# Performance work log

Measured on AMD Instinct MI355X. Metric: run time of the kernel, lower is better.

The kernel has to match this reference:

```python
import jax, jax.numpy as jnp
import numpy as np

N_NODES = 8000
N_EDGES = 64000
HEADS = 8
OUT_C = 512
NEG_SLOPE = 0.2
EPS = 1e-16


def setup_inputs() -> dict:
    key = jax.random.key(0)
    ks = jax.random.split(key, 8)
    x = jax.random.normal(ks[0], (N_NODES, 128), dtype=jnp.float32)
    edge_index = jax.random.randint(ks[1], (2, N_EDGES), 0, N_NODES, dtype=jnp.int64)
    W_gat = jax.random.normal(ks[2], (128, HEADS * OUT_C), dtype=jnp.float32) * 0.05
    b_gat = jax.random.normal(ks[3], (HEADS * OUT_C,), dtype=jnp.float32) * 0.05
    att_src = jax.random.normal(ks[4], (HEADS, OUT_C), dtype=jnp.float32) * 0.05
    att_dst = jax.random.normal(ks[5], (HEADS, OUT_C), dtype=jnp.float32) * 0.05
    W_lin = jax.random.normal(ks[6], (HEADS * OUT_C, 512), dtype=jnp.float32) * 0.02
    b_lin = jax.random.normal(ks[7], (512,), dtype=jnp.float32) * 0.02
    return {"x": x, "edge_index": edge_index, "W_gat": W_gat, "b_gat": b_gat,
            "att_src": att_src, "att_dst": att_dst, "W_lin": W_lin, "b_lin": b_lin}


def reference(x, edge_index, W_gat, b_gat, att_src, att_dst, W_lin, b_lin):
    N = x.shape[0]
    # shared linear projection (PyG GATConv single-tensor input): [N, H, C]
    h = (x @ W_gat).reshape(N, HEADS, OUT_C)
    # add self loops (PyG default add_self_loops=True)
    loop = jnp.arange(N, dtype=edge_index.dtype)
    src = jnp.concatenate([edge_index[0], loop])  # source j
    dst = jnp.concatenate([edge_index[1], loop])  # destination i
    # per-node attention logits: [N, H]
    a_src = jnp.einsum('nhc,hc->nh', h, att_src)
    a_dst = jnp.einsum('nhc,hc->nh', h, att_dst)
    # edge logits, leaky relu
    e = jax.nn.leaky_relu(a_src[src] + a_dst[dst], NEG_SLOPE)  # [E, H]
    # softmax over edges sharing a destination
    emax = jax.ops.segment_max(e, dst, num_segments=N)
    ez = jnp.exp(e - emax[dst])
    denom = jax.ops.segment_sum(ez, dst, num_segments=N)
    alpha = ez / (denom[dst] + EPS)  # [E, H]
    # weighted scatter-add of source features
    msg = h[src] * alpha[:, :, None]  # [E, H, C]
    agg = jax.ops.segment_sum(msg, dst, num_segments=N)  # [N, H, C]
    gat_out = agg.reshape(N, HEADS * OUT_C) + b_gat
    return gat_out @ W_lin + b_lin
```

## Files before the change

kernel.cpp:

```cpp
#include <hip/hip_runtime.h>
#include <hip/hip_bf16.h>

#define NN   8000
#define NE   64000
#define NE2  72000
#define NH   8
#define OC   512
#define HC   4096
#define KIN  128
#define NOUT 512
#define YW   1024
#define MAXDEG 64
#define NEG_SLOPE 0.2f

#define VSRC_NB   128
#define PHA_NB    129

#define PB_GEMM_NB 64
#define FILL_BASE  64
#define BEFF_BASE  346
#define ATT_BASE   362
#define PHB_NB     862

#define GEMM_NB   500

using bf16 = __hip_bfloat16;
typedef float  f32x4  __attribute__((ext_vector_type(4)));
typedef __bf16 bf16x8 __attribute__((ext_vector_type(8)));

static __device__ __forceinline__ void gld_lds16(const bf16* g, bf16* l){
    __builtin_amdgcn_global_load_lds(
        (const __attribute__((address_space(1))) unsigned int*)g,
        (__attribute__((address_space(3))) unsigned int*)l, 16, 0, 0);
}

struct Acc24 { f32x4 a[2][4]; };

static __device__ __forceinline__ void gemm64x128_bk64(
    const bf16* __restrict__ A, int lda, const bf16* __restrict__ BT, int ldb,
    int K, bf16* sA, bf16* sB, int tid, Acc24& acc)
{
    const int lane = tid & 63;
    const int w    = tid >> 6;
    const int wm   = w >> 1, wn = w & 1;
    const int m16  = lane & 15, q = lane >> 4;

    const int cA0 = tid,        cA1 = tid + 256;
    const int rA0 = cA0 >> 3,   jA0 = (cA0 & 7) ^ (rA0 & 7);
    const int rA1 = cA1 >> 3,   jA1 = (cA1 & 7) ^ (rA1 & 7);
    const size_t gA0 = (size_t)rA0 * lda + jA0 * 8;
    const size_t gA1 = (size_t)rA1 * lda + jA1 * 8;
    size_t gB[4]; int cB[4];
    #pragma unroll
    for (int u=0; u<4; ++u){
        int c = tid + 256*u;
        int r = c >> 3, j = (c & 7) ^ (r & 7);
        cB[u] = c;
        gB[u] = (size_t)r * ldb + j * 8;
    }

    #pragma unroll
    for (int i=0;i<2;++i)
        #pragma unroll
        for (int j=0;j<4;++j)
            #pragma unroll
            for (int r=0;r<4;++r) acc.a[i][j][r] = 0.f;

    gld_lds16(A  + gA0, sA + cA0*8);
    gld_lds16(A  + gA1, sA + cA1*8);
    #pragma unroll
    for (int u=0; u<4; ++u) gld_lds16(BT + gB[u], sB + cB[u]*8);
    __syncthreads();

    const int nIter = K / 64;
    for (int it = 0; it < nIter; ++it){
        const int cur = it & 1, nxt = cur ^ 1;
        bf16x8 af[2][2], bfr[4][2];
        #pragma unroll
        for (int ks=0; ks<2; ++ks){
            #pragma unroll
            for (int i=0;i<2;++i){
                int row = wm*32 + i*16 + m16;
                int p   = (ks*4 + q) ^ (row & 7);
                af[i][ks] = *(const bf16x8*)(const void*)(sA + cur*64*64 + row*64 + p*8);
            }
            #pragma unroll
            for (int j=0;j<4;++j){
                int row = wn*64 + j*16 + m16;
                int p   = (ks*4 + q) ^ (row & 7);
                bfr[j][ks] = *(const bf16x8*)(const void*)(sB + cur*128*64 + row*64 + p*8);
            }
        }
        if (it + 1 < nIter){
            const size_t ko = (size_t)(it+1) * 64;
            gld_lds16(A  + gA0 + ko, sA + nxt*64*64 + cA0*8);
            gld_lds16(A  + gA1 + ko, sA + nxt*64*64 + cA1*8);
            #pragma unroll
            for (int u=0; u<4; ++u) gld_lds16(BT + gB[u] + ko, sB + nxt*128*64 + cB[u]*8);
        }
        #pragma unroll
        for (int ks=0; ks<2; ++ks)
            #pragma unroll
            for (int i=0;i<2;++i)
                #pragma unroll
                for (int j=0;j<4;++j)
                    acc.a[i][j] = __builtin_amdgcn_mfma_f32_16x16x32_bf16(af[i][ks], bfr[j][ks], acc.a[i][j], 0, 0, 0);
        __syncthreads();
    }
}

__global__ __launch_bounds__(256) void k_phaseA(
    const float* __restrict__ W_gat,
    const float* __restrict__ att_src, const float* __restrict__ att_dst,
    bf16* __restrict__ Wg, float* __restrict__ v,
    int* __restrict__ cursors)
{
    const int bid = blockIdx.x;
    const int tid = threadIdx.x;

    if (bid < VSRC_NB){
        int k = bid;
        int lane = tid & 63, g = tid >> 6;
        for (int hh = g; hh < NH; hh += 4){
            const float* wp = W_gat + (size_t)k*HC + hh*OC;
            bf16*        wb = Wg    + (size_t)k*HC + hh*OC;
            const float* as = att_src + hh*OC;
            const float* ad = att_dst + hh*OC;
            float ss = 0.f, sd = 0.f;
            #pragma unroll
            for (int c0=0; c0<OC; c0+=64){
                float wv = wp[c0+lane];
                wb[c0+lane] = __float2bfloat16(wv);
                ss = fmaf(wv, as[c0+lane], ss);
                sd = fmaf(wv, ad[c0+lane], sd);
            }
            #pragma unroll
            for (int off=32; off; off>>=1){
                ss += __shfl_down(ss, off);
                sd += __shfl_down(sd, off);
            }
            if (lane == 0){
                v[k*16 + hh]     = ss;
                v[k*16 + 8 + hh] = sd;
            }
        }
    } else {
        for (int i = tid*4; i < NN; i += 1024){
            int4 z; z.x = z.y = z.z = z.w = 0;
            *reinterpret_cast<int4*>(cursors + i) = z;
        }
    }
}

__global__ __launch_bounds__(256) void k_phaseB(
    const bf16* __restrict__ Wg, const float* __restrict__ W_lin,
    const float* __restrict__ b_gat, const int* __restrict__ eidx,
    bf16* __restrict__ WcT, float* __restrict__ beff_part,
    int* __restrict__ cursors, int* __restrict__ esrc,
    const float* __restrict__ x, const float* __restrict__ v,
    float* __restrict__ a_src, float* __restrict__ a_dst)
{
    __shared__ __align__(16) char smem_raw[16*132*2*4];
    const int bid = blockIdx.x;
    const int tid = threadIdx.x;

    if (bid < PB_GEMM_NB){
        bf16* sA = (bf16*)smem_raw;
        bf16* sB = (bf16*)smem_raw + 64*32;

        const int head = bid >> 3;
        const int rem  = bid & 7;
        const int m0   = (rem >> 2) * 64;
        const int n0   = (rem & 3) * 128;
        const int lane = tid & 63;
        const int w = tid >> 6, wm = w >> 1, wn = w & 1;
        const int m16 = lane & 15, q = lane >> 4;

        const int rA = tid >> 2, kA = (tid & 3) * 8;
        const bf16* Abase = Wg + (size_t)(m0 + rA)*HC + head*OC + kA;

        f32x4 acc[2][4];
        #pragma unroll
        for (int i=0;i<2;++i)
            #pragma unroll
            for (int j=0;j<4;++j)
                #pragma unroll
                for (int r=0;r<4;++r) acc[i][j][r] = 0.f;

        for (int kc = 0; kc < OC; kc += 32){
            __syncthreads();
            gld_lds16(Abase + kc, sA + tid*8);
            #pragma unroll
            for (int u=0; u<4; ++u){
                int idx = tid*4 + u;
                int r    = idx >> 5;
                int gcol = (idx & 31) * 4;
                const float* src = W_lin + (size_t)(head*OC + kc + r)*NOUT + n0 + gcol;
                float4 vv = *(const float4*)src;
                sB[(gcol+0)*32 + r] = __float2bfloat16(vv.x);
                sB[(gcol+1)*32 + r] = __float2bfloat16(vv.y);
                sB[(gcol+2)*32 + r] = __float2bfloat16(vv.z);
                sB[(gcol+3)*32 + r] = __float2bfloat16(vv.w);
            }
            __syncthreads();
            bf16x8 af[2], bfr[4];
            #pragma unroll
            for (int i=0;i<2;++i)
                af[i]  = *(const bf16x8*)(const void*)(sA + ((wm*32 + i*16 + m16)*32 + q*8));
            #pragma unroll
            for (int j=0;j<4;++j)
                bfr[j] = *(const bf16x8*)(const void*)(sB + ((wn*64 + j*16 + m16)*32 + q*8));
            #pragma unroll
            for (int i=0;i<2;++i)
                #pragma unroll
                for (int j=0;j<4;++j)
                    acc[i][j] = __builtin_amdgcn_mfma_f32_16x16x32_bf16(af[i], bfr[j], acc[i][j], 0, 0, 0);
        }

        #pragma unroll
        for (int i=0;i<2;++i){
            int row_base = m0 + wm*32 + i*16 + q*4;
            #pragma unroll
            for (int j=0;j<4;++j){
                int col = n0 + wn*64 + j*16 + m16;
                ushort4 pk;
                bf16 b0 = __float2bfloat16(acc[i][j][0]);
                bf16 b1 = __float2bfloat16(acc[i][j][1]);
                bf16 b2 = __float2bfloat16(acc[i][j][2]);
                bf16 b3 = __float2bfloat16(acc[i][j][3]);
                pk.x = *(unsigned short*)&b0; pk.y = *(unsigned short*)&b1;
                pk.z = *(unsigned short*)&b2; pk.w = *(unsigned short*)&b3;
                *reinterpret_cast<ushort4*>(WcT + (size_t)col*YW + head*KIN + row_base) = pk;
            }
        }
        return;
    }

    if (bid < BEFF_BASE){
        int e = (bid - FILL_BASE)*256 + tid;
        if (e < NE2){
            int src, dst;
            if (e < NE){ src = eidx[e]; dst = eidx[NE+e]; } else { src = dst = e - NE; }
            int pos = atomicAdd(&cursors[dst], 1);
            if (pos < MAXDEG) esrc[dst*MAXDEG + pos] = src;
        }
        return;
    }

    if (bid < ATT_BASE){
        int b = bid - BEFF_BASE;
        int o = tid * 2;
        const float* bg = b_gat + b*256;
        const float* wl = W_lin + (size_t)b*256*NOUT + o;
        float a0 = 0.f, a1 = 0.f;
        #pragma unroll 4
        for (int r=0; r<256; ++r){
            float bv = bg[r];
            float2 wv = *(const float2*)(wl + (size_t)r*NOUT);
            a0 = fmaf(bv, wv.x, a0);
            a1 = fmaf(bv, wv.y, a1);
        }
        beff_part[b*NOUT + o]     = a0;
        beff_part[b*NOUT + o + 1] = a1;
        return;
    }

    float (*xs)[132] = (float(*)[132])smem_raw;
    float (*vt)[132] = (float(*)[132])(smem_raw + 16*132*4);
    int node0 = (bid - ATT_BASE) * 16;
    {
        const float* xg = x + (size_t)node0*KIN;
        int row = tid >> 4, co = (tid & 15) * 8;
        float4 v0 = *(const float4*)(xg + row*KIN + co);
        float4 v1 = *(const float4*)(xg + row*KIN + co + 4);
        *(float4*)&xs[row][co]     = v0;
        *(float4*)&xs[row][co + 4] = v1;
    }
    {
        int base = tid*8;
        #pragma unroll
        for (int j=0;j<8;++j){
            int idx = base + j;
            vt[idx & 15][idx >> 4] = v[idx];
        }
    }
    __syncthreads();
    int ln = tid >> 4, o = tid & 15;
    float acc = 0.f;
    #pragma unroll
    for (int k0=0;k0<KIN;k0+=4){
        float4 xv = *(const float4*)&xs[ln][k0];
        float4 vv = *(const float4*)&vt[o][k0];
        acc += xv.x*vv.x + xv.y*vv.y + xv.z*vv.z + xv.w*vv.w;
    }
    int node = node0 + ln;
    if (o < 8) a_src[node*NH + o]     = acc;
    else       a_dst[node*NH + o - 8] = acc;
}

__global__ __launch_bounds__(256) void k_agg(const int* __restrict__ cnts,
    const int* __restrict__ esrc, const float* __restrict__ a_src,
    const float* __restrict__ a_dst, const float* __restrict__ x,
    bf16* __restrict__ Y)
{
    int node = blockIdx.x*4 + (threadIdx.x >> 6);
    int lane = threadIdx.x & 63;
    int s0 = node*MAXDEG, s1 = s0 + min(cnts[node], MAXDEG);
    int g = lane >> 3, h = lane & 7;
    float adl = a_dst[node*NH + h];
    float m = -1e30f, sum = 0.f;
    for (int e = s0 + g; e < s1; e += 8){
        float l = a_src[esrc[e]*NH + h] + adl;
        l = l > 0.f ? l : NEG_SLOPE*l;
        float mn = fmaxf(m, l);
        sum = sum*__expf(m - mn) + __expf(l - mn);
        m = mn;
    }
    #pragma unroll
    for (int d=8; d<64; d<<=1){
        float mo = __shfl_xor(m, d);
        float so = __shfl_xor(sum, d);
        float mn = fmaxf(m, mo);
        sum = sum*__expf(m - mn) + so*__expf(mo - mn);
        m = mn;
    }
    float inv = 1.f / (sum + 1e-16f);
    float acc[16];
    #pragma unroll
    for (int j=0;j<16;++j) acc[j] = 0.f;

    int src_n = esrc[s0];
    float2 xv_n = *(const float2*)(x + (size_t)src_n*KIN + lane*2);
    float al_n = (lane < 8) ? a_src[src_n*NH + lane] : 0.f;
    for (int s = s0; s < s1; ++s){
        float2 xv = xv_n;
        float al = al_n;
        if (s + 1 < s1){
            int sn = esrc[s+1];
            xv_n = *(const float2*)(x + (size_t)sn*KIN + lane*2);
            al_n = (lane < 8) ? a_src[sn*NH + lane] : 0.f;
        }
        float wl = 0.f;
        if (lane < 8){
            float l = al + adl;
            l = l > 0.f ? l : NEG_SLOPE*l;
            wl = __expf(l - m) * inv;
        }
        #pragma unroll
        for (int hh=0; hh<8; ++hh){
            float wh = __shfl(wl, hh);
            acc[hh*2]   = fmaf(wh, xv.x, acc[hh*2]);
            acc[hh*2+1] = fmaf(wh, xv.y, acc[hh*2+1]);
        }
    }
    bf16* yp = Y + (size_t)node*YW + lane*2;
    #pragma unroll
    for (int hh=0; hh<8; ++hh){
        bf16 b0 = __float2bfloat16(acc[hh*2]);
        bf16 b1 = __float2bfloat16(acc[hh*2+1]);
        ushort2 pk;
        pk.x = *(unsigned short*)&b0;
        pk.y = *(unsigned short*)&b1;
        *reinterpret_cast<ushort2*>(yp + hh*KIN) = pk;
    }
}

__global__ __launch_bounds__(256) void k_gemm64(
    const bf16* __restrict__ A, const bf16* __restrict__ BT,
    const float* __restrict__ beff_part, const float* __restrict__ b_lin,
    float* __restrict__ C)
{
    __shared__ __align__(16) bf16 sA[2*64*64];
    __shared__ __align__(16) bf16 sB[2*128*64];
    const int tid = threadIdx.x;

    const int orig = blockIdx.x;
    const int xcd = orig & 7, slot = orig >> 3;
    const int wgid = (xcd < 4 ? xcd*63 : 252 + (xcd-4)*62) + slot;
    const int m0 = (wgid >> 2) * 64;
    const int n0 = (wgid & 3) * 128;

    Acc24 acc;
    gemm64x128_bk64(A + (size_t)m0*YW, YW, BT + (size_t)n0*YW, YW, YW, sA, sB, tid, acc);

    const int lane = tid & 63;
    const int w = tid >> 6, wm = w >> 1, wn = w & 1;
    const int m16 = lane & 15, q = lane >> 4;
    #pragma unroll
    for (int j=0;j<4;++j){
        int col = n0 + wn*64 + j*16 + m16;
        float bval = b_lin[col];
        #pragma unroll
        for (int p=0;p<16;++p) bval += beff_part[p*NOUT + col];
        #pragma unroll
        for (int i=0;i<2;++i){
            int row_base = m0 + wm*32 + i*16 + q*4;
            #pragma unroll
            for (int r=0;r<4;++r)
                C[(size_t)(row_base + r)*NOUT + col] = acc.a[i][j][r] + bval;
        }
    }
}

extern "C" void kernel_launch(void* const* d_in, const int* in_sizes, int n_in,
                              void* d_out, int out_size, void* d_ws, size_t ws_size,
                              hipStream_t stream)
{
    const float* x       = (const float*)d_in[0];
    const int*   eidx    = (const int*)  d_in[1];
    const float* W_gat   = (const float*)d_in[2];
    const float* b_gat   = (const float*)d_in[3];
    const float* att_src = (const float*)d_in[4];
    const float* att_dst = (const float*)d_in[5];
    const float* W_lin   = (const float*)d_in[6];
    const float* b_lin   = (const float*)d_in[7];
    float* out = (float*)d_out;

    char* p = (char*)d_ws;
    auto alloc = [&](size_t bytes){ void* r = (void*)p; p += (bytes + 255) & ~(size_t)255; return r; };
    bf16*  Wg        = (bf16*) alloc((size_t)KIN*HC*2);
    bf16*  WcT       = (bf16*) alloc((size_t)NOUT*YW*2);
    bf16*  Ybuf      = (bf16*) alloc((size_t)NN*YW*2);
    float* v         = (float*)alloc((size_t)KIN*16*4);
    float* a_src     = (float*)alloc((size_t)NN*NH*4);
    float* a_dst     = (float*)alloc((size_t)NN*NH*4);
    int*   esrc      = (int*)  alloc((size_t)NN*MAXDEG*4);
    int*   cursors   = (int*)  alloc((size_t)NN*4);
    float* beff_part = (float*)alloc((size_t)16*NOUT*4);
    if ((size_t)(p - (char*)d_ws) > ws_size) return;

    k_phaseA<<<PHA_NB, 256, 0, stream>>>(W_gat, att_src, att_dst, Wg, v, cursors);
    k_phaseB<<<PHB_NB, 256, 0, stream>>>(Wg, W_lin, b_gat, eidx, WcT, beff_part,
                                         cursors, esrc, x, v, a_src, a_dst);
    k_agg<<<NN/4, 256, 0, stream>>>(cursors, esrc, a_src, a_dst, x, Ybuf);
    k_gemm64<<<GEMM_NB, 256, 0, stream>>>(Ybuf, WcT, beff_part, b_lin, out);
}
```

Measured before the change: 136.1 us.

## Pre-transpose W_lin to bf16 in phase A and double-buffer weight-fold GEMM

Phase A gains 128 blocks that tile W_lin through LDS, write a transposed bf16 copy (WlT), and compute per-block partial bias products. The phase B weight-fold GEMM then streams both operands with direct global-to-LDS loads into a double-buffered, XOR-swizzled LDS layout. Before, each k-step did strided fp32 loads and scalar transposed LDS stores. A single reducer block now collapses the 128 bias partials, so the final GEMM epilogue reads one bias vector instead of summing 16 partials. The cost is an extra 4 MB intermediate buffer and additional work in phase A.

```diff
diff --git a/kernel.cpp b/kernel.cpp
--- a/kernel.cpp
+++ b/kernel.cpp
@@ -14,13 +14,14 @@
 #define NEG_SLOPE 0.2f
 
 #define VSRC_NB   128
-#define PHA_NB    129
+#define TRN_BASE  129
+#define PHA_NB    257
 
 #define PB_GEMM_NB 64
 #define FILL_BASE  64
-#define BEFF_BASE  346
-#define ATT_BASE   362
-#define PHB_NB     862
+#define RED_BID    346
+#define ATT_BASE   347
+#define PHB_NB     847
 
 #define GEMM_NB   500
 
@@ -112,9 +113,13 @@
 __global__ __launch_bounds__(256) void k_phaseA(
     const float* __restrict__ W_gat,
     const float* __restrict__ att_src, const float* __restrict__ att_dst,
+    const float* __restrict__ W_lin, const float* __restrict__ b_gat,
     bf16* __restrict__ Wg, float* __restrict__ v,
+    bf16* __restrict__ WlT, float* __restrict__ beff_part,
     int* __restrict__ cursors)
 {
+    __shared__ float tl[32][132];
+    __shared__ float bg_s[32];
     const int bid = blockIdx.x;
     const int tid = threadIdx.x;
 
@@ -144,29 +149,66 @@
                 v[k*16 + 8 + hh] = sd;
             }
         }
-    } else {
+    } else if (bid == VSRC_NB){
         for (int i = tid*4; i < NN; i += 1024){
             int4 z; z.x = z.y = z.z = z.w = 0;
             *reinterpret_cast<int4*>(cursors + i) = z;
         }
+    } else {
+        int b = bid - TRN_BASE;
+        if (tid < 32) bg_s[tid] = b_gat[b*32 + tid];
+        for (int sub = 0; sub < 4; ++sub){
+            __syncthreads();
+            #pragma unroll
+            for (int u = 0; u < 4; ++u){
+                int f = tid + 256*u;
+                int row = f >> 5;
+                int cq  = f & 31;
+                float4 vv = *(const float4*)(W_lin + (size_t)(b*32+row)*NOUT + sub*128 + cq*4);
+                *(float4*)&tl[row][cq*4] = vv;
+            }
+            __syncthreads();
+            if (tid < 128){
+                float a = 0.f;
+                #pragma unroll
+                for (int c = 0; c < 32; ++c) a = fmaf(bg_s[c], tl[c][tid], a);
+                beff_part[(size_t)b*NOUT + sub*128 + tid] = a;
+            }
+            {
+                int o_loc = tid >> 1, half = tid & 1;
+                unsigned int us[8];
+                #pragma unroll
+                for (int k = 0; k < 8; ++k){
+                    float v0 = tl[half*16 + 2*k][o_loc];
+                    float v1 = tl[half*16 + 2*k + 1][o_loc];
+                    bf16 b0 = __float2bfloat16(v0), b1 = __float2bfloat16(v1);
+                    us[k] = (unsigned int)*(unsigned short*)&b0
+                          | ((unsigned int)*(unsigned short*)&b1 << 16);
+                }
+                bf16* dst = WlT + (size_t)(sub*128 + o_loc)*HC + b*32 + half*16;
+                *(uint4*)(dst)     = *(uint4*)&us[0];
+                *(uint4*)(dst + 8) = *(uint4*)&us[4];
+            }
+        }
     }
 }
 
 __global__ __launch_bounds__(256) void k_phaseB(
-    const bf16* __restrict__ Wg, const float* __restrict__ W_lin,
-    const float* __restrict__ b_gat, const int* __restrict__ eidx,
-    bf16* __restrict__ WcT, float* __restrict__ beff_part,
+    const bf16* __restrict__ Wg, const bf16* __restrict__ WlT,
+    const int* __restrict__ eidx,
+    bf16* __restrict__ WcT,
+    const float* __restrict__ beff_part, float* __restrict__ beff,
     int* __restrict__ cursors, int* __restrict__ esrc,
     const float* __restrict__ x, const float* __restrict__ v,
     float* __restrict__ a_src, float* __restrict__ a_dst)
 {
-    __shared__ __align__(16) char smem_raw[16*132*2*4];
+    __shared__ __align__(16) char smem_raw[24576];
     const int bid = blockIdx.x;
     const int tid = threadIdx.x;
 
     if (bid < PB_GEMM_NB){
         bf16* sA = (bf16*)smem_raw;
-        bf16* sB = (bf16*)smem_raw + 64*32;
+        bf16* sB = (bf16*)smem_raw + 2*64*32;
 
         const int head = bid >> 3;
         const int rem  = bid & 7;
@@ -176,8 +218,12 @@
         const int w = tid >> 6, wm = w >> 1, wn = w & 1;
         const int m16 = lane & 15, q = lane >> 4;
 
-        const int rA = tid >> 2, kA = (tid & 3) * 8;
-        const bf16* Abase = Wg + (size_t)(m0 + rA)*HC + head*OC + kA;
+        const int rA = tid >> 2, jA = (tid & 3) ^ (rA & 3);
+        const bf16* Asrc = Wg + (size_t)(m0 + rA)*HC + head*OC + jA*8;
+        const int rB0 = tid >> 2,         jB0 = (tid & 3) ^ (rB0 & 3);
+        const int rB1 = (tid + 256) >> 2, jB1 = ((tid + 256) & 3) ^ (rB1 & 3);
+        const bf16* Bsrc0 = WlT + (size_t)(n0 + rB0)*HC + head*OC + jB0*8;
+        const bf16* Bsrc1 = WlT + (size_t)(n0 + rB1)*HC + head*OC + jB1*8;
 
         f32x4 acc[2][4];
         #pragma unroll
@@ -187,34 +233,39 @@
                 #pragma unroll
                 for (int r=0;r<4;++r) acc[i][j][r] = 0.f;
 
-        for (int kc = 0; kc < OC; kc += 32){
-            __syncthreads();
-            gld_lds16(Abase + kc, sA + tid*8);
-            #pragma unroll
-            for (int u=0; u<4; ++u){
-                int idx = tid*4 + u;
-                int r    = idx >> 5;
-                int gcol = (idx & 31) * 4;
-                const float* src = W_lin + (size_t)(head*OC + kc + r)*NOUT + n0 + gcol;
-                float4 vv = *(const float4*)src;
-                sB[(gcol+0)*32 + r] = __float2bfloat16(vv.x);
-                sB[(gcol+1)*32 + r] = __float2bfloat16(vv.y);
-                sB[(gcol+2)*32 + r] = __float2bfloat16(vv.z);
-                sB[(gcol+3)*32 + r] = __float2bfloat16(vv.w);
-            }
-            __syncthreads();
+        gld_lds16(Asrc,  sA + tid*8);
+        gld_lds16(Bsrc0, sB + tid*8);
+        gld_lds16(Bsrc1, sB + (tid+256)*8);
+        __syncthreads();
+
+        const int nIter = OC / 32;
+        for (int it = 0; it < nIter; ++it){
+            const int cur = it & 1, nxt = cur ^ 1;
             bf16x8 af[2], bfr[4];
             #pragma unroll
-            for (int i=0;i<2;++i)
-                af[i]  = *(const bf16x8*)(const void*)(sA + ((wm*32 + i*16 + m16)*32 + q*8));
-            #pragma unroll
-            for (int j=0;j<4;++j)
-                bfr[j] = *(const bf16x8*)(const void*)(sB + ((wn*64 + j*16 + m16)*32 + q*8));
+            for (int i=0;i<2;++i){
+                int row = wm*32 + i*16 + m16;
+                int p   = q ^ (row & 3);
+                af[i] = *(const bf16x8*)(const void*)(sA + cur*64*32 + row*32 + p*8);
+            }
+            #pragma unroll
+            for (int j=0;j<4;++j){
+                int row = wn*64 + j*16 + m16;
+                int p   = q ^ (row & 3);
+                bfr[j] = *(const bf16x8*)(const void*)(sB + cur*128*32 + row*32 + p*8);
+            }
+            if (it + 1 < nIter){
+                int ko = (it+1) * 32;
+                gld_lds16(Asrc  + ko, sA + nxt*64*32 + tid*8);
+                gld_lds16(Bsrc0 + ko, sB + nxt*128*32 + tid*8);
+                gld_lds16(Bsrc1 + ko, sB + nxt*128*32 + (tid+256)*8);
+            }
             #pragma unroll
             for (int i=0;i<2;++i)
                 #pragma unroll
                 for (int j=0;j<4;++j)
                     acc[i][j] = __builtin_amdgcn_mfma_f32_16x16x32_bf16(af[i], bfr[j], acc[i][j], 0, 0, 0);
+            __syncthreads();
         }
 
         #pragma unroll
@@ -236,7 +287,7 @@
         return;
     }
 
-    if (bid < BEFF_BASE){
+    if (bid < RED_BID){
         int e = (bid - FILL_BASE)*256 + tid;
         if (e < NE2){
             int src, dst;
@@ -247,21 +298,14 @@
         return;
     }
 
-    if (bid < ATT_BASE){
-        int b = bid - BEFF_BASE;
+    if (bid == RED_BID){
         int o = tid * 2;
-        const float* bg = b_gat + b*256;
-        const float* wl = W_lin + (size_t)b*256*NOUT + o;
-        float a0 = 0.f, a1 = 0.f;
-        #pragma unroll 4
-        for (int r=0; r<256; ++r){
-            float bv = bg[r];
-            float2 wv = *(const float2*)(wl + (size_t)r*NOUT);
-            a0 = fmaf(bv, wv.x, a0);
-            a1 = fmaf(bv, wv.y, a1);
-        }
-        beff_part[b*NOUT + o]     = a0;
-        beff_part[b*NOUT + o + 1] = a1;
+        float s0 = 0.f, s1 = 0.f;
+        for (int b = 0; b < 128; ++b){
+            float2 vv = *(const float2*)(beff_part + (size_t)b*NOUT + o);
+            s0 += vv.x; s1 += vv.y;
+        }
+        beff[o] = s0; beff[o+1] = s1;
         return;
     }
 
@@ -367,7 +411,7 @@
 
 __global__ __launch_bounds__(256) void k_gemm64(
     const bf16* __restrict__ A, const bf16* __restrict__ BT,
-    const float* __restrict__ beff_part, const float* __restrict__ b_lin,
+    const float* __restrict__ beff, const float* __restrict__ b_lin,
     float* __restrict__ C)
 {
     __shared__ __align__(16) bf16 sA[2*64*64];
@@ -389,9 +433,7 @@
     #pragma unroll
     for (int j=0;j<4;++j){
         int col = n0 + wn*64 + j*16 + m16;
-        float bval = b_lin[col];
-        #pragma unroll
-        for (int p=0;p<16;++p) bval += beff_part[p*NOUT + col];
+        float bval = beff[col] + b_lin[col];
         #pragma unroll
         for (int i=0;i<2;++i){
             int row_base = m0 + wm*32 + i*16 + q*4;
@@ -419,6 +461,7 @@
     char* p = (char*)d_ws;
     auto alloc = [&](size_t bytes){ void* r = (void*)p; p += (bytes + 255) & ~(size_t)255; return r; };
     bf16*  Wg        = (bf16*) alloc((size_t)KIN*HC*2);
+    bf16*  WlT       = (bf16*) alloc((size_t)NOUT*HC*2);
     bf16*  WcT       = (bf16*) alloc((size_t)NOUT*YW*2);
     bf16*  Ybuf      = (bf16*) alloc((size_t)NN*YW*2);
     float* v         = (float*)alloc((size_t)KIN*16*4);
@@ -426,12 +469,14 @@
     float* a_dst     = (float*)alloc((size_t)NN*NH*4);
     int*   esrc      = (int*)  alloc((size_t)NN*MAXDEG*4);
     int*   cursors   = (int*)  alloc((size_t)NN*4);
-    float* beff_part = (float*)alloc((size_t)16*NOUT*4);
+    float* beff_part = (float*)alloc((size_t)128*NOUT*4);
+    float* beff      = (float*)alloc((size_t)NOUT*4);
     if ((size_t)(p - (char*)d_ws) > ws_size) return;
 
-    k_phaseA<<<PHA_NB, 256, 0, stream>>>(W_gat, att_src, att_dst, Wg, v, cursors);
-    k_phaseB<<<PHB_NB, 256, 0, stream>>>(Wg, W_lin, b_gat, eidx, WcT, beff_part,
+    k_phaseA<<<PHA_NB, 256, 0, stream>>>(W_gat, att_src, att_dst, W_lin, b_gat,
+                                         Wg, v, WlT, beff_part, cursors);
+    k_phaseB<<<PHB_NB, 256, 0, stream>>>(Wg, WlT, eidx, WcT, beff_part, beff,
                                          cursors, esrc, x, v, a_src, a_dst);
     k_agg<<<NN/4, 256, 0, stream>>>(cursors, esrc, a_src, a_dst, x, Ybuf);
-    k_gemm64<<<GEMM_NB, 256, 0, stream>>>(Ybuf, WcT, beff_part, b_lin, out);
-}
+    k_gemm64<<<GEMM_NB, 256, 0, stream>>>(Ybuf, WcT, beff, b_lin, out);
+}
```

Result: faster. 127.0 us (-6.7%).
